# Optimization experiments

Hardware: AMD Instinct MI355X
Metric: run time of the kernel (lower is better)

## Reference

```python
import jax, jax.numpy as jnp
import numpy as np

B, T, HID = 2, 2048, 2048
NH, NKV, D = 16, 4, 128
WIN = 512
ROPE_BASE = 10000.0
SCALE = D ** -0.5
EPS = 1e-12


def setup_inputs() -> dict:
    key = jax.random.key(0)
    ks = jax.random.split(key, 5)
    x = jax.random.normal(ks[0], (B, T, HID), dtype=jnp.float32)
    wq = jax.random.normal(ks[1], (HID, NH * D), dtype=jnp.float32) * 0.02
    wk = jax.random.normal(ks[2], (HID, NKV * D), dtype=jnp.float32) * 0.02
    wv = jax.random.normal(ks[3], (HID, NKV * D), dtype=jnp.float32) * 0.02
    wo = jax.random.normal(ks[4], (NH * D, HID), dtype=jnp.float32) * 0.02
    return {"x": x, "wq": wq, "wk": wk, "wv": wv, "wo": wo}


def _rope_tables(t, offset=0):
    inv_freq = 1.0 / (ROPE_BASE ** (jnp.arange(0, D, 2, dtype=jnp.float32) / D))
    pos = jnp.arange(offset, offset + t, dtype=jnp.float32)
    freqs = pos[:, None] * inv_freq[None, :]              # [t, D/2]
    cos = jnp.concatenate([jnp.cos(freqs), jnp.cos(freqs)], axis=-1)  # [t, D]
    sin = jnp.concatenate([jnp.sin(freqs), jnp.sin(freqs)], axis=-1)
    return cos, sin


def _apply_rope(x, cos, sin):
    # x: [B, H, T, D]; rotate-half formulation
    x1, x2 = jnp.split(x, 2, axis=-1)
    rot = jnp.concatenate([-x2, x1], axis=-1)
    return x * cos[None, None] + rot * sin[None, None]


def _l2norm(x):
    n = jnp.sqrt(jnp.sum(x * x, axis=-1, keepdims=True))
    return x / jnp.maximum(n, EPS)


def _forward(x, wq, wk, wv, wo):
    b, t, _ = x.shape
    q = (x @ wq).reshape(b, t, NH, D).transpose(0, 2, 1, 3)    # [B,H,T,D]
    k = (x @ wk).reshape(b, t, NKV, D).transpose(0, 2, 1, 3)   # [B,Hk,T,D]
    v = (x @ wv).reshape(b, t, NKV, D).transpose(0, 2, 1, 3)
    q = _l2norm(q)
    k = _l2norm(k)
    cos, sin = _rope_tables(t, offset=0)
    q = _apply_rope(q, cos, sin)
    k = _apply_rope(k, cos, sin)
    rep = NH // NKV
    k = jnp.repeat(k, rep, axis=1)                             # GQA repeat_interleave
    v = jnp.repeat(v, rep, axis=1)
    i = jnp.arange(t)
    allowed = (i[None, :] <= i[:, None]) & (i[None, :] > i[:, None] - WIN)  # [T,T]
    logits = jnp.einsum("bhid,bhjd->bhij", q, k) * SCALE
    logits = jnp.where(allowed[None, None], logits, -jnp.inf)
    attn = jax.nn.softmax(logits, axis=-1)
    out = jnp.einsum("bhij,bhjd->bhid", attn, v)
    out = out.transpose(0, 2, 1, 3).reshape(b, t, NH * D)
    return out @ wo


def reference(x, wq, wk, wv, wo):
    return _forward(x, wq, wk, wv, wo)
```

## Files before the change

kernel.cpp:

```cpp
#include <hip/hip_runtime.h>
#include <hip/hip_bf16.h>
#include <cstdint>

#define NHQ 16
#define NKVH 4
#define HDIM 128
#define WINSZ 512
#define TSEQ 2048
#define ATTN_SCALE 0.08838834764831845f

typedef __attribute__((ext_vector_type(8))) short s16x8;
typedef __attribute__((ext_vector_type(4))) float f32x4;

__device__ __forceinline__ void gload16(const void* g, void* lds) {
  __builtin_amdgcn_global_load_lds(
      (const __attribute__((address_space(1))) unsigned int*)g,
      (__attribute__((address_space(3))) unsigned int*)(uintptr_t)lds,
      16, 0, 0);
}

__device__ __forceinline__ f32x4 mfma16(s16x8 a, s16x8 b, f32x4 c) {
  return __builtin_amdgcn_mfma_f32_16x16x32_bf16(a, b, c, 0, 0, 0);
}

#define SBAR() asm volatile("s_barrier" ::: "memory")
#define VMCNT(n) asm volatile("s_waitcnt vmcnt(" #n ")" ::: "memory")
#define LGKM(n) asm volatile("s_waitcnt lgkmcnt(" #n ")" ::: "memory")

__global__ __launch_bounds__(256) void rope_tables_kernel(float* __restrict__ cosT,
                                                          float* __restrict__ sinT) {
  int idx = blockIdx.x * 256 + threadIdx.x;
  int t = idx >> 6, d2 = idx & 63;
  float inv = powf(10000.0f, -(float)d2 / 64.0f);
  float a = (float)t * inv;
  cosT[idx] = cosf(a);
  sinT[idx] = sinf(a);
}

__global__ __launch_bounds__(256) void cast_kernel(const float* __restrict__ in,
                                                   __bf16* __restrict__ out, int n4) {
  int i = blockIdx.x * 256 + threadIdx.x;
  if (i >= n4) return;
  float4 v = ((const float4*)in)[i];
  union { __bf16 h[4]; uint2 u; } pk;
  pk.h[0] = (__bf16)v.x; pk.h[1] = (__bf16)v.y; pk.h[2] = (__bf16)v.z; pk.h[3] = (__bf16)v.w;
  ((uint2*)out)[i] = pk.u;
}

__global__ __launch_bounds__(256) void transpose_cast(const float* __restrict__ in,
                                                      __bf16* __restrict__ out, int R, int C) {
  __shared__ float tile[32][33];
  int c0 = blockIdx.x * 32, r0 = blockIdx.y * 32;
  int tx = threadIdx.x, ty = threadIdx.y;
#pragma unroll
  for (int i = 0; i < 4; i++)
    tile[ty + i * 8][tx] = in[(size_t)(r0 + ty + i * 8) * C + c0 + tx];
  __syncthreads();
#pragma unroll
  for (int i = 0; i < 4; i++)
    out[(size_t)(c0 + ty + i * 8) * R + r0 + tx] = (__bf16)tile[tx][ty + i * 8];
}

template <int MODE>
__global__ __launch_bounds__(512, 2) void gemm8(const __bf16* __restrict__ A,
                                                const __bf16* __restrict__ Bt,
                                                float* __restrict__ Cf,
                                                __bf16* __restrict__ Qo, __bf16* __restrict__ Ko,
                                                __bf16* __restrict__ Vo, int M, int N, int K) {
  __shared__ __attribute__((aligned(16))) char Lds[2][65536];

  const int tid = threadIdx.x;
  const int w = tid >> 6, lane = tid & 63;
  const int wm = w >> 2, wn = w & 3;

  const int nbx = gridDim.x;
  const int nwg = nbx * gridDim.y;
  const int bid = blockIdx.y * nbx + blockIdx.x;
  const int q8 = nwg >> 3, r8 = nwg & 7;
  const int xcd = bid & 7, idx = bid >> 3;
  const int swz = (xcd < r8 ? xcd * (q8 + 1) : r8 * (q8 + 1) + (xcd - r8) * q8) + idx;
  const int bx = swz % nbx, by = swz / nbx;
  const int m0 = by * 256, n0 = bx * 256;

  const int ru = tid >> 3;
  const int cs = (tid & 7) ^ (ru & 7);
  const __bf16* gAs = A + (size_t)(m0 + ru) * K + cs * 8;
  const __bf16* gBs = Bt + (size_t)(n0 + ru) * K + cs * 8;

  auto stA = [&](int tt, int u) {
    gload16(gAs + (size_t)(64 * u) * K + tt * 64, Lds[tt & 1] + u * 8192 + w * 1024);
  };
  auto stB = [&](int tt, int u) {
    gload16(gBs + (size_t)(64 * u) * K + tt * 64, Lds[tt & 1] + 32768 + u * 8192 + w * 1024);
  };

  const int rowb = (lane & 15) * 128;
  const int cph0 = (((lane >> 4)) ^ (lane & 7)) * 16;
  const int cph1 = ((4 + (lane >> 4)) ^ (lane & 7)) * 16;
  const int Abase = wm * 16384;
  const int Bbase = 32768 + wn * 8192;

  f32x4 acc[8][4];
  f32x4 zero = {0.f, 0.f, 0.f, 0.f};
#pragma unroll
  for (int i = 0; i < 8; i++)
#pragma unroll
    for (int j = 0; j < 4; j++) acc[i][j] = zero;

  const int NT = K >> 6;

#pragma unroll
  for (int u = 0; u < 4; u++) stA(0, u);
#pragma unroll
  for (int u = 0; u < 4; u++) stB(0, u);
#pragma unroll
  for (int u = 0; u < 4; u++) stA(1, u);
#pragma unroll
  for (int u = 0; u < 4; u++) stB(1, u);
  VMCNT(8);
  SBAR();

  s16x8 fa[4][2], fb[4][2];

  for (int t = 0; t < NT; ++t) {
    const char* bs = Lds[t & 1];
    const bool more = (t + 2) < NT;

#pragma unroll
    for (int mi = 0; mi < 4; mi++) {
      fa[mi][0] = *(const s16x8*)(bs + Abase + mi * 2048 + rowb + cph0);
      fa[mi][1] = *(const s16x8*)(bs + Abase + mi * 2048 + rowb + cph1);
    }
#pragma unroll
    for (int ni = 0; ni < 2; ni++) {
      fb[ni][0] = *(const s16x8*)(bs + Bbase + ni * 2048 + rowb + cph0);
      fb[ni][1] = *(const s16x8*)(bs + Bbase + ni * 2048 + rowb + cph1);
    }
    SBAR();
    LGKM(0);
    __builtin_amdgcn_sched_barrier(0);
    __builtin_amdgcn_s_setprio(1);
#pragma unroll
    for (int mi = 0; mi < 4; mi++)
#pragma unroll
      for (int ni = 0; ni < 2; ni++)
#pragma unroll
        for (int kk = 0; kk < 2; kk++)
          acc[mi][ni] = mfma16(fa[mi][kk], fb[ni][kk], acc[mi][ni]);
    __builtin_amdgcn_s_setprio(0);
    SBAR();

#pragma unroll
    for (int ni = 2; ni < 4; ni++) {
      fb[ni][0] = *(const s16x8*)(bs + Bbase + ni * 2048 + rowb + cph0);
      fb[ni][1] = *(const s16x8*)(bs + Bbase + ni * 2048 + rowb + cph1);
    }
    if (more) { stA(t + 2, 0); stA(t + 2, 2); }
    SBAR();
    LGKM(0);
    __builtin_amdgcn_sched_barrier(0);
    __builtin_amdgcn_s_setprio(1);
#pragma unroll
    for (int mi = 0; mi < 4; mi++)
#pragma unroll
      for (int ni = 2; ni < 4; ni++)
#pragma unroll
        for (int kk = 0; kk < 2; kk++)
          acc[mi][ni] = mfma16(fa[mi][kk], fb[ni][kk], acc[mi][ni]);
    __builtin_amdgcn_s_setprio(0);
    SBAR();

#pragma unroll
    for (int mi = 0; mi < 4; mi++) {
      fa[mi][0] = *(const s16x8*)(bs + Abase + 8192 + mi * 2048 + rowb + cph0);
      fa[mi][1] = *(const s16x8*)(bs + Abase + 8192 + mi * 2048 + rowb + cph1);
    }
    if (more) { stB(t + 2, 0); stB(t + 2, 1); stB(t + 2, 2); stB(t + 2, 3); }
    SBAR();
    LGKM(0);
    __builtin_amdgcn_sched_barrier(0);
    __builtin_amdgcn_s_setprio(1);
#pragma unroll
    for (int mi = 0; mi < 4; mi++)
#pragma unroll
      for (int ni = 0; ni < 2; ni++)
#pragma unroll
        for (int kk = 0; kk < 2; kk++)
          acc[4 + mi][ni] = mfma16(fa[mi][kk], fb[ni][kk], acc[4 + mi][ni]);
    __builtin_amdgcn_s_setprio(0);
    SBAR();

    if (more) { stA(t + 2, 1); stA(t + 2, 3); }
    if (t + 2 < NT) {
      VMCNT(8);
    } else if (t + 1 < NT) {
      VMCNT(0);
    }
    SBAR();
    __builtin_amdgcn_s_setprio(1);
#pragma unroll
    for (int mi = 0; mi < 4; mi++)
#pragma unroll
      for (int ni = 2; ni < 4; ni++)
#pragma unroll
        for (int kk = 0; kk < 2; kk++)
          acc[4 + mi][ni] = mfma16(fa[mi][kk], fb[ni][kk], acc[4 + mi][ni]);
    __builtin_amdgcn_s_setprio(0);
    SBAR();
  }

#pragma unroll
  for (int mf = 0; mf < 8; mf++)
#pragma unroll
    for (int nf = 0; nf < 4; nf++) {
      int rbase = m0 + wm * 128 + mf * 16 + (lane >> 4) * 4;
      int col = n0 + wn * 64 + nf * 16 + (lane & 15);
#pragma unroll
      for (int r = 0; r < 4; r++) {
        int m = rbase + r;
        float v = acc[mf][nf][r];
        if constexpr (MODE == 0) {
          Cf[(size_t)m * N + col] = v;
        } else {
          int b = m >> 11, tq = m & 2047;
          __bf16 bv = (__bf16)v;
          if (col < 2048) {
            Qo[(((size_t)(b * NHQ + (col >> 7))) * TSEQ + tq) * HDIM + (col & 127)] = bv;
          } else if (col < 2560) {
            int c2 = col - 2048;
            Ko[(((size_t)(b * NKVH + (c2 >> 7))) * TSEQ + tq) * HDIM + (c2 & 127)] = bv;
          } else {
            int c2 = col - 2560;
            Vo[(((size_t)(b * NKVH + (c2 >> 7))) * TSEQ + tq) * HDIM + (c2 & 127)] = bv;
          }
        }
      }
    }
}

__global__ __launch_bounds__(256) void normrope(__bf16* __restrict__ Q, __bf16* __restrict__ Kk,
                                                const float* __restrict__ cosT,
                                                const float* __restrict__ sinT) {
  int w = threadIdx.x >> 6, lane = threadIdx.x & 63;
  int row = blockIdx.x / 5;
  int slot = (blockIdx.x % 5) * 4 + w;
  int b = row >> 11, t = row & 2047;
  __bf16* p;
  if (slot < 16)
    p = Q + (((size_t)(b * NHQ + slot)) * TSEQ + t) * HDIM;
  else
    p = Kk + (((size_t)(b * NKVH + (slot - 16))) * TSEQ + t) * HDIM;
  float x1 = (float)p[lane], x2 = (float)p[lane + 64];
  float ss = x1 * x1 + x2 * x2;
#pragma unroll
  for (int off = 32; off; off >>= 1) ss += __shfl_xor(ss, off);
  float inv = 1.0f / fmaxf(sqrtf(ss), 1e-12f);
  x1 *= inv;
  x2 *= inv;
  float c = cosT[t * 64 + lane], s = sinT[t * 64 + lane];
  p[lane] = (__bf16)(x1 * c - x2 * s);
  p[lane + 64] = (__bf16)(x2 * c + x1 * s);
}

__global__ __launch_bounds__(1024) void attn_kernel(const __bf16* __restrict__ Qf,
                                                    const __bf16* __restrict__ Kf,
                                                    const __bf16* __restrict__ Vf,
                                                    __bf16* __restrict__ Ab) {
  __shared__ __attribute__((aligned(16))) char KlB[64 * 256];
  __shared__ __attribute__((aligned(16))) char VtB[128 * 128];
  __shared__ __attribute__((aligned(16))) char PlB[16 * 2048];
  int tid = threadIdx.x, w = tid >> 6, lane = tid & 63;
  int bid = blockIdx.x;
  int qt = bid & 31, kvh = (bid >> 5) & 3, b = bid >> 7;
  int qs = qt * 64;
  int h = kvh * 4 + (w >> 2);
  int wr = w & 3;
  const __bf16* Qb = Qf + ((size_t)(b * NHQ + h) * TSEQ) * HDIM;
  const __bf16* Kb = Kf + ((size_t)(b * NKVH + kvh) * TSEQ) * HDIM;
  const __bf16* Vb = Vf + ((size_t)(b * NKVH + kvh) * TSEQ) * HDIM;
  char* Pw = PlB + w * 2048;

  s16x8 aq[4];
  int qrow_f = qs + wr * 16 + (lane & 15);
#pragma unroll
  for (int kb = 0; kb < 4; kb++)
    aq[kb] = *(const s16x8*)(Qb + (size_t)qrow_f * HDIM + kb * 32 + (lane >> 4) * 8);

  f32x4 acc[8];
  f32x4 zero = {0.f, 0.f, 0.f, 0.f};
#pragma unroll
  for (int db = 0; db < 8; db++) acc[db] = zero;
  float mrow[4], lrow[4];
#pragma unroll
  for (int r = 0; r < 4; r++) { mrow[r] = -1e30f; lrow[r] = 0.f; }

  int lo = qs - (WINSZ - 1);
  if (lo < 0) lo = 0;
  lo &= ~63;
  const int nt = ((qs + 64) - lo) >> 6;

  const int kjrow = tid >> 4, kkc = tid & 15;
  const int vk = tid & 63, vd0 = (tid >> 6) * 8;

  int4 kE, vE, kO, vO;

#define ATTN_LOAD(KR, VR, KS)                                                      \
  {                                                                                \
    KR = *(const int4*)(Kb + (size_t)((KS) + kjrow) * HDIM + kkc * 8);             \
    VR = *(const int4*)(Vb + (size_t)((KS) + vk) * HDIM + vd0);                    \
  }

#define ATTN_WRITE(KR, VR)                                                         \
  {                                                                                \
    *(int4*)(KlB + kjrow * 256 + ((kkc * 16) ^ ((kjrow & 7) << 4))) = KR;          \
    const __bf16* pv = (const __bf16*)&VR;                                         \
    _Pragma("unroll") for (int e = 0; e < 8; e++) {                                \
      int d = vd0 + e;                                                             \
      *(__bf16*)(VtB + d * 128 + ((vk * 2) ^ ((d & 7) << 4))) = pv[e];             \
    }                                                                              \
  }

#define ATTN_COMPUTE(KS)                                                           \
  {                                                                                \
    f32x4 sacc[4];                                                                 \
    _Pragma("unroll") for (int jb = 0; jb < 4; jb++) sacc[jb] = zero;              \
    _Pragma("unroll") for (int jb = 0; jb < 4; jb++) {                             \
      int key = jb * 16 + (lane & 15);                                             \
      _Pragma("unroll") for (int kb = 0; kb < 4; kb++) {                           \
        s16x8 bk = *(const s16x8*)(KlB + key * 256 +                               \
                                   ((kb * 64 + (lane >> 4) * 16) ^ ((key & 7) << 4))); \
        sacc[jb] = mfma16(aq[kb], bk, sacc[jb]);                                   \
      }                                                                            \
    }                                                                              \
    float scf[4];                                                                  \
    _Pragma("unroll") for (int r = 0; r < 4; r++) {                                \
      int qrow = qs + wr * 16 + (lane >> 4) * 4 + r;                               \
      float sv[4]; bool av[4];                                                     \
      _Pragma("unroll") for (int jb = 0; jb < 4; jb++) {                           \
        int j = (KS) + jb * 16 + (lane & 15);                                      \
        av[jb] = (j <= qrow) && (j > qrow - WINSZ);                                \
        sv[jb] = sacc[jb][r] * ATTN_SCALE;                                         \
      }                                                                            \
      float mt = -1e30f;                                                           \
      _Pragma("unroll") for (int jb = 0; jb < 4; jb++)                             \
        mt = fmaxf(mt, av[jb] ? sv[jb] : -1e30f);                                  \
      _Pragma("unroll") for (int off = 1; off < 16; off <<= 1)                     \
        mt = fmaxf(mt, __shfl_xor(mt, off));                                       \
      float mn = fmaxf(mrow[r], mt);                                               \
      float pv_[4]; float ts = 0.f;                                                \
      _Pragma("unroll") for (int jb = 0; jb < 4; jb++) {                           \
        pv_[jb] = av[jb] ? __expf(sv[jb] - mn) : 0.f;                              \
        ts += pv_[jb];                                                             \
      }                                                                            \
      _Pragma("unroll") for (int off = 1; off < 16; off <<= 1)                     \
        ts += __shfl_xor(ts, off);                                                 \
      float sf = __expf(mrow[r] - mn);                                             \
      lrow[r] = lrow[r] * sf + ts;                                                 \
      mrow[r] = mn;                                                                \
      scf[r] = sf;                                                                 \
      int q = (lane >> 4) * 4 + r;                                                 \
      _Pragma("unroll") for (int jb = 0; jb < 4; jb++)                             \
        *(__bf16*)(Pw + q * 128 +                                                  \
                   (((jb * 16 + (lane & 15)) * 2) ^ ((q & 7) << 4))) = (__bf16)pv_[jb]; \
    }                                                                              \
    s16x8 pa[2];                                                                   \
    _Pragma("unroll") for (int kb = 0; kb < 2; kb++) {                             \
      int q = lane & 15;                                                           \
      pa[kb] = *(const s16x8*)(Pw + q * 128 +                                      \
                               ((kb * 64 + (lane >> 4) * 16) ^ ((q & 7) << 4)));   \
    }                                                                              \
    _Pragma("unroll") for (int db = 0; db < 8; db++) {                             \
      f32x4 tt = acc[db];                                                          \
      _Pragma("unroll") for (int r = 0; r < 4; r++) tt[r] *= scf[r];               \
      acc[db] = tt;                                                                \
    }                                                                              \
    _Pragma("unroll") for (int db = 0; db < 8; db++) {                             \
      int d = db * 16 + (lane & 15);                                               \
      _Pragma("unroll") for (int kb = 0; kb < 2; kb++) {                           \
        s16x8 bv = *(const s16x8*)(VtB + d * 128 +                                 \
                                   ((kb * 64 + (lane >> 4) * 16) ^ ((d & 7) << 4))); \
        acc[db] = mfma16(pa[kb], bv, acc[db]);                                     \
      }                                                                            \
    }                                                                              \
  }

  int ks = lo;
  ATTN_LOAD(kE, vE, ks);
  int it = 0;
  for (; it + 2 <= nt; it += 2) {
    ATTN_WRITE(kE, vE);
    ATTN_LOAD(kO, vO, ks + 64);
    __syncthreads();
    ATTN_COMPUTE(ks);
    __syncthreads();
    ks += 64;
    ATTN_WRITE(kO, vO);
    if (it + 2 < nt) ATTN_LOAD(kE, vE, ks + 64);
    __syncthreads();
    ATTN_COMPUTE(ks);
    __syncthreads();
    ks += 64;
  }
  if (it < nt) {
    ATTN_WRITE(kE, vE);
    __syncthreads();
    ATTN_COMPUTE(ks);
  }

#undef ATTN_LOAD
#undef ATTN_WRITE
#undef ATTN_COMPUTE

#pragma unroll
  for (int db = 0; db < 8; db++)
#pragma unroll
    for (int r = 0; r < 4; r++) {
      int qrow = qs + wr * 16 + (lane >> 4) * 4 + r;
      float v = acc[db][r] / lrow[r];
      Ab[((size_t)(b * TSEQ + qrow)) * 2048 + h * HDIM + db * 16 + (lane & 15)] = (__bf16)v;
    }
}

extern "C" void kernel_launch(void* const* d_in, const int* in_sizes, int n_in,
                              void* d_out, int out_size, void* d_ws, size_t ws_size,
                              hipStream_t stream) {
  const float* x = (const float*)d_in[0];
  const float* wq = (const float*)d_in[1];
  const float* wk = (const float*)d_in[2];
  const float* wv = (const float*)d_in[3];
  const float* wo = (const float*)d_in[4];
  float* out = (float*)d_out;

  char* ws = (char*)d_ws;
  size_t off = 0;
  auto alloc = [&](size_t bytes) -> void* {
    void* p = ws + off;
    off += (bytes + 255) & ~(size_t)255;
    return p;
  };
  __bf16* Xb = (__bf16*)alloc((size_t)4096 * 2048 * 2);
  __bf16* Wqkvt = (__bf16*)alloc((size_t)3072 * 2048 * 2);
  __bf16* Wot = (__bf16*)alloc((size_t)2048 * 2048 * 2);
  __bf16* Q = (__bf16*)alloc((size_t)2 * NHQ * TSEQ * HDIM * 2);
  __bf16* Kb = (__bf16*)alloc((size_t)2 * NKVH * TSEQ * HDIM * 2);
  __bf16* Vb = (__bf16*)alloc((size_t)2 * NKVH * TSEQ * HDIM * 2);
  float* cosT = (float*)alloc((size_t)TSEQ * 64 * 4);
  float* sinT = (float*)alloc((size_t)TSEQ * 64 * 4);
  __bf16* Ab = Xb;

  rope_tables_kernel<<<TSEQ * 64 / 256, 256, 0, stream>>>(cosT, sinT);
  cast_kernel<<<8192, 256, 0, stream>>>(x, Xb, 2097152);
  dim3 tb(32, 8);
  transpose_cast<<<dim3(64, 64), tb, 0, stream>>>(wq, Wqkvt, 2048, 2048);
  transpose_cast<<<dim3(16, 64), tb, 0, stream>>>(wk, Wqkvt + (size_t)2048 * 2048, 2048, 512);
  transpose_cast<<<dim3(16, 64), tb, 0, stream>>>(wv, Wqkvt + (size_t)2560 * 2048, 2048, 512);
  transpose_cast<<<dim3(64, 64), tb, 0, stream>>>(wo, Wot, 2048, 2048);

  gemm8<1><<<dim3(12, 16), 512, 0, stream>>>(Xb, Wqkvt, nullptr, Q, Kb, Vb, 4096, 3072, 2048);
  normrope<<<4096 * 5, 256, 0, stream>>>(Q, Kb, cosT, sinT);
  attn_kernel<<<2 * NKVH * (TSEQ / 64), 1024, 0, stream>>>(Q, Kb, Vb, Ab);
  gemm8<0><<<dim3(8, 16), 512, 0, stream>>>(Ab, Wot, out, nullptr, nullptr, nullptr, 4096, 2048,
                                            2048);
}
```

Measured before the change: 255.5 us.

## Split attention blocks per query head instead of sharing KV tiles across GQA group

The attention kernel now launches one 256-thread block per (batch, query head, 64-row tile) instead of one 1024-thread block per KV head that served all four query heads. Each thread loads four K/V chunks per tile, and the double-buffer loop is simplified into a single loop with alternating register sets. The intent is smaller blocks with less LDS (smaller P buffer), more blocks per CU, and cheaper barriers. The cost is that each K/V tile is loaded and transposed into LDS four times, once per query head, instead of once per GQA group.

```diff
diff --git a/kernel.cpp b/kernel.cpp
--- a/kernel.cpp
+++ b/kernel.cpp
@@ -262,26 +262,25 @@
   p[lane + 64] = (__bf16)(x2 * c + x1 * s);
 }
 
-__global__ __launch_bounds__(1024) void attn_kernel(const __bf16* __restrict__ Qf,
-                                                    const __bf16* __restrict__ Kf,
-                                                    const __bf16* __restrict__ Vf,
-                                                    __bf16* __restrict__ Ab) {
+__global__ __launch_bounds__(256) void attn_kernel(const __bf16* __restrict__ Qf,
+                                                   const __bf16* __restrict__ Kf,
+                                                   const __bf16* __restrict__ Vf,
+                                                   __bf16* __restrict__ Ab) {
   __shared__ __attribute__((aligned(16))) char KlB[64 * 256];
   __shared__ __attribute__((aligned(16))) char VtB[128 * 128];
-  __shared__ __attribute__((aligned(16))) char PlB[16 * 2048];
+  __shared__ __attribute__((aligned(16))) char PlB[4 * 2048];
   int tid = threadIdx.x, w = tid >> 6, lane = tid & 63;
   int bid = blockIdx.x;
-  int qt = bid & 31, kvh = (bid >> 5) & 3, b = bid >> 7;
+  int qt = bid & 31, h = (bid >> 5) & 15, b = bid >> 9;
   int qs = qt * 64;
-  int h = kvh * 4 + (w >> 2);
-  int wr = w & 3;
+  int kvh = h >> 2;
   const __bf16* Qb = Qf + ((size_t)(b * NHQ + h) * TSEQ) * HDIM;
   const __bf16* Kb = Kf + ((size_t)(b * NKVH + kvh) * TSEQ) * HDIM;
   const __bf16* Vb = Vf + ((size_t)(b * NKVH + kvh) * TSEQ) * HDIM;
   char* Pw = PlB + w * 2048;
 
   s16x8 aq[4];
-  int qrow_f = qs + wr * 16 + (lane & 15);
+  int qrow_f = qs + w * 16 + (lane & 15);
 #pragma unroll
   for (int kb = 0; kb < 4; kb++)
     aq[kb] = *(const s16x8*)(Qb + (size_t)qrow_f * HDIM + kb * 32 + (lane >> 4) * 8);
@@ -299,23 +298,25 @@
   lo &= ~63;
   const int nt = ((qs + 64) - lo) >> 6;
 
-  const int kjrow = tid >> 4, kkc = tid & 15;
-  const int vk = tid & 63, vd0 = (tid >> 6) * 8;
-
-  int4 kE, vE, kO, vO;
+  const int kjr = tid >> 4, kkc = tid & 15;
+  const int vk = tid & 63, vg = tid >> 6;
+
+  int4 kA[4], vA[4], kB[4], vB[4];
 
 #define ATTN_LOAD(KR, VR, KS)                                                      \
-  {                                                                                \
-    KR = *(const int4*)(Kb + (size_t)((KS) + kjrow) * HDIM + kkc * 8);             \
-    VR = *(const int4*)(Vb + (size_t)((KS) + vk) * HDIM + vd0);                    \
+  _Pragma("unroll") for (int i = 0; i < 4; i++) {                                  \
+    KR[i] = *(const int4*)(Kb + (size_t)((KS) + kjr + 16 * i) * HDIM + kkc * 8);   \
+    VR[i] = *(const int4*)(Vb + (size_t)((KS) + vk) * HDIM + (vg + 4 * i) * 8);    \
   }
 
 #define ATTN_WRITE(KR, VR)                                                         \
-  {                                                                                \
-    *(int4*)(KlB + kjrow * 256 + ((kkc * 16) ^ ((kjrow & 7) << 4))) = KR;          \
-    const __bf16* pv = (const __bf16*)&VR;                                         \
+  _Pragma("unroll") for (int i = 0; i < 4; i++) {                                  \
+    int jr = kjr + 16 * i;                                                         \
+    *(int4*)(KlB + jr * 256 + ((kkc * 16) ^ ((jr & 7) << 4))) = KR[i];             \
+    const __bf16* pv = (const __bf16*)&VR[i];                                      \
+    int d0 = (vg + 4 * i) * 8;                                                     \
     _Pragma("unroll") for (int e = 0; e < 8; e++) {                                \
-      int d = vd0 + e;                                                             \
+      int d = d0 + e;                                                              \
       *(__bf16*)(VtB + d * 128 + ((vk * 2) ^ ((d & 7) << 4))) = pv[e];             \
     }                                                                              \
   }
@@ -334,7 +335,7 @@
     }                                                                              \
     float scf[4];                                                                  \
     _Pragma("unroll") for (int r = 0; r < 4; r++) {                                \
-      int qrow = qs + wr * 16 + (lane >> 4) * 4 + r;                               \
+      int qrow = qs + w * 16 + (lane >> 4) * 4 + r;                                \
       float sv[4]; bool av[4];                                                     \
       _Pragma("unroll") for (int jb = 0; jb < 4; jb++) {                           \
         int j = (KS) + jb * 16 + (lane & 15);                                      \
@@ -385,27 +386,20 @@
   }
 
   int ks = lo;
-  ATTN_LOAD(kE, vE, ks);
-  int it = 0;
-  for (; it + 2 <= nt; it += 2) {
-    ATTN_WRITE(kE, vE);
-    ATTN_LOAD(kO, vO, ks + 64);
-    __syncthreads();
-    ATTN_COMPUTE(ks);
-    __syncthreads();
-    ks += 64;
-    ATTN_WRITE(kO, vO);
-    if (it + 2 < nt) ATTN_LOAD(kE, vE, ks + 64);
+  ATTN_LOAD(kA, vA, lo);
+  for (int t = 0; t < nt; ++t) {
+    if ((t & 1) == 0) {
+      ATTN_WRITE(kA, vA);
+      if (t + 1 < nt) ATTN_LOAD(kB, vB, ks + 64);
+    } else {
+      ATTN_WRITE(kB, vB);
+      if (t + 1 < nt) ATTN_LOAD(kA, vA, ks + 64);
+    }
     __syncthreads();
     ATTN_COMPUTE(ks);
     __syncthreads();
     ks += 64;
   }
-  if (it < nt) {
-    ATTN_WRITE(kE, vE);
-    __syncthreads();
-    ATTN_COMPUTE(ks);
-  }
 
 #undef ATTN_LOAD
 #undef ATTN_WRITE
@@ -415,7 +409,7 @@
   for (int db = 0; db < 8; db++)
 #pragma unroll
     for (int r = 0; r < 4; r++) {
-      int qrow = qs + wr * 16 + (lane >> 4) * 4 + r;
+      int qrow = qs + w * 16 + (lane >> 4) * 4 + r;
       float v = acc[db][r] / lrow[r];
       Ab[((size_t)(b * TSEQ + qrow)) * 2048 + h * HDIM + db * 16 + (lane & 15)] = (__bf16)v;
     }
@@ -458,7 +452,7 @@
 
   gemm8<1><<<dim3(12, 16), 512, 0, stream>>>(Xb, Wqkvt, nullptr, Q, Kb, Vb, 4096, 3072, 2048);
   normrope<<<4096 * 5, 256, 0, stream>>>(Q, Kb, cosT, sinT);
-  attn_kernel<<<2 * NKVH * (TSEQ / 64), 1024, 0, stream>>>(Q, Kb, Vb, Ab);
+  attn_kernel<<<2 * NHQ * (TSEQ / 64), 256, 0, stream>>>(Q, Kb, Vb, Ab);
   gemm8<0><<<dim3(8, 16), 512, 0, stream>>>(Ab, Wot, out, nullptr, nullptr, nullptr, 4096, 2048,
                                             2048);
 }
```

Measured after the change: 242.7 us. -5.0%, faster.
